# Kernel tuning notes

Hardware: AMD Instinct MI355X
Metric: run time of the kernel (lower is better)

The kernel has to match this reference:

```python
import jax, jax.numpy as jnp
import numpy as np
from jax import lax

T_STEPS = 10       # fixed unroll length in forward (range(10))
TASK = 16          # params['task_size']
FEAT = 256         # input_size - task_size
VOCAB = 128        # params['vocab_size']
SH = 512           # sender_hidden_size
RH = 512           # receiver_hidden_size
ND = 10            # num_digits
B = 16384          # batch_size


def _gru_step(h, x, Wih, Whh, bih, bhh):
    # PyTorch GRU/GRUCell equations. Wih: [3H, In], Whh: [3H, H]
    gi = x @ Wih.T + bih
    gh = h @ Whh.T + bhh
    ir, iz, inn = jnp.split(gi, 3, axis=-1)
    hr, hz, hn = jnp.split(gh, 3, axis=-1)
    r = jax.nn.sigmoid(ir + hr)
    z = jax.nn.sigmoid(iz + hz)
    n = jnp.tanh(inn + r * hn)
    return (1.0 - z) * n + z * h


def setup_inputs() -> dict:
    key = jax.random.key(0)
    ks = jax.random.split(key, 16)
    s = 0.05
    x = jax.random.normal(ks[0], (B, TASK + FEAT), jnp.float32)
    u = jax.random.uniform(ks[1], (T_STEPS, B, VOCAB), jnp.float32, 1e-6, 1.0 - 1e-6)
    gumbel = -jnp.log(-jnp.log(u))  # standard Gumbel noise, fixed for determinism
    inp = {
        "x": x,
        "gumbel": gumbel,
        "W_in": jax.random.normal(ks[2], (SH, FEAT), jnp.float32) * s,
        "b_in": jnp.zeros((SH,), jnp.float32),
        "Wih_s": jax.random.normal(ks[3], (3 * SH, VOCAB), jnp.float32) * s,
        "Whh_s": jax.random.normal(ks[4], (3 * SH, SH), jnp.float32) * s,
        "bih_s": jnp.zeros((3 * SH,), jnp.float32),
        "bhh_s": jnp.zeros((3 * SH,), jnp.float32),
        "W_sp": jax.random.normal(ks[5], (VOCAB, SH), jnp.float32) * s,
        "b_sp": jnp.zeros((VOCAB,), jnp.float32),
        "Wih_r": jax.random.normal(ks[6], (3 * RH, VOCAB), jnp.float32) * s,
        "Whh_r": jax.random.normal(ks[7], (3 * RH, RH), jnp.float32) * s,
        "bih_r": jnp.zeros((3 * RH,), jnp.float32),
        "bhh_r": jnp.zeros((3 * RH,), jnp.float32),
        "W_c": jax.random.normal(ks[8], (ND, RH + TASK), jnp.float32) * s,
        "b_c": jnp.zeros((ND,), jnp.float32),
    }
    return inp


def _forward(x, gumbel, W_in, b_in, Wih_s, Whh_s, bih_s, bhh_s, W_sp, b_sp,
             Wih_r, Whh_r, bih_r, bhh_r, W_c, b_c):
    feats = x[:, TASK:]
    task = x[:, :TASK]
    h0 = jnp.tanh(feats @ W_in.T + b_in)                      # [B, SH]
    inp0 = jnp.zeros((x.shape[0], VOCAB), x.dtype)

    def sender_step(carry, g):
        h, w = carry
        h = _gru_step(h, w, Wih_s, Whh_s, bih_s, bhh_s)
        logits = h @ W_sp.T + b_sp
        y_soft = jax.nn.softmax(logits + g, axis=-1)          # gumbel_softmax, tau=1
        onehot = jax.nn.one_hot(jnp.argmax(y_soft, axis=-1), VOCAB, dtype=y_soft.dtype)
        y = onehot + y_soft - lax.stop_gradient(y_soft)       # hard straight-through
        return (h, lax.stop_gradient(y)), y                   # input_word = y.detach()

    (_, _), output_words = lax.scan(sender_step, (h0, inp0), gumbel)  # [10, B, V]

    # cumulative stop-token masking: once argmax==0 at step i-1, zero all steps >= i
    words = jnp.argmax(output_words, axis=2)                  # [10, B]
    nz = (words != 0).astype(output_words.dtype)
    alive = jnp.concatenate(
        [jnp.ones((1, words.shape[1]), output_words.dtype), jnp.cumprod(nz[:-1], axis=0)],
        axis=0)                                               # [10, B]
    masked = output_words * alive[:, :, None]

    # receiver GRU, zero initial hidden, return final hidden
    hr0 = jnp.zeros((x.shape[0], RH), x.dtype)

    def recv_step(h, w):
        h = _gru_step(h, w, Wih_r, Whh_r, bih_r, bhh_r)
        return h, None

    h_n, _ = lax.scan(recv_step, hr0, masked)                 # [B, RH]
    score = jnp.concatenate([h_n, task], axis=1) @ W_c.T + b_c  # [B, ND]
    return score


def reference(x, gumbel, W_in, b_in, Wih_s, Whh_s, bih_s, bhh_s, W_sp, b_sp,
              Wih_r, Whh_r, bih_r, bhh_r, W_c, b_c):
    return _forward(x, gumbel, W_in, b_in, Wih_s, Whh_s, bih_s, bhh_s, W_sp, b_sp,
                    Wih_r, Whh_r, bih_r, bhh_r, W_c, b_c)
```

## Files before the change

kernel.cpp:

```cpp
#include <hip/hip_runtime.h>
#include <math.h>

#define NB 16384
#define NT 10
#define CHM 8192

typedef _Float16 f16;
typedef f16 f16x8 __attribute__((ext_vector_type(8)));
typedef f16 f16x4 __attribute__((ext_vector_type(4)));
typedef float f32x4 __attribute__((ext_vector_type(4)));

__device__ __forceinline__ float sigm(float v) { return 1.0f / (1.0f + expf(-v)); }

__global__ __launch_bounds__(256) void h0_kernel(
    const float* __restrict__ x, const float* __restrict__ W,
    const float* __restrict__ bias, f16* __restrict__ h_hi, f16* __restrict__ h_lo)
{
    __shared__ __align__(16) float As[32][128];
    __shared__ __align__(16) float Ws[32][64];
    const int t = threadIdx.x;
    const int tx = t & 15, ty = t >> 4;
    const int mBase = blockIdx.x * 128, nBase = blockIdx.y * 64;
    const int kq = (t & 7) * 4, r8 = t >> 3;

    float4 acc[8];
    #pragma unroll
    for (int mi = 0; mi < 8; ++mi) acc[mi] = make_float4(0.f, 0.f, 0.f, 0.f);

    const float* aPtr = x + (size_t)(mBase + r8) * 272 + 16 + kq;
    const float* wPtr = W + (size_t)(nBase + r8) * 256 + kq;

    for (int kb = 0; kb < 8; ++kb) {
        const int k0 = kb * 32;
        __syncthreads();
        #pragma unroll
        for (int i = 0; i < 4; ++i) {
            float4 v = *(const float4*)(aPtr + (size_t)(i * 32) * 272 + k0);
            const int row = r8 + i * 32;
            const float vv[4] = {v.x, v.y, v.z, v.w};
            #pragma unroll
            for (int j = 0; j < 4; ++j) As[kq + j][row ^ ((kq + j) & 28)] = vv[j];
        }
        #pragma unroll
        for (int i = 0; i < 2; ++i) {
            float4 v = *(const float4*)(wPtr + (size_t)(i * 32) * 256 + k0);
            const int row = r8 + i * 32;
            const float vv[4] = {v.x, v.y, v.z, v.w};
            #pragma unroll
            for (int j = 0; j < 4; ++j) Ws[kq + j][row ^ ((kq + j) & 28)] = vv[j];
        }
        __syncthreads();
        #pragma unroll 8
        for (int k = 0; k < 32; ++k) {
            const int s = k & 28;
            float4 a0 = *(const float4*)&As[k][(ty * 8) ^ s];
            float4 a1 = *(const float4*)&As[k][((ty * 8) + 4) ^ s];
            float4 bb = *(const float4*)&Ws[k][(tx * 4) ^ s];
            const float am[8] = {a0.x, a0.y, a0.z, a0.w, a1.x, a1.y, a1.z, a1.w};
            #pragma unroll
            for (int mi = 0; mi < 8; ++mi) {
                acc[mi].x += am[mi] * bb.x; acc[mi].y += am[mi] * bb.y;
                acc[mi].z += am[mi] * bb.z; acc[mi].w += am[mi] * bb.w;
            }
        }
    }
    const int j0 = nBase + tx * 4;
    const int kg = j0 >> 3, jo = j0 & 7;
    const float4 b4 = *(const float4*)&bias[j0];
    #pragma unroll
    for (int mi = 0; mi < 8; ++mi) {
        const int row = mBase + ty * 8 + mi;
        float o[4];
        o[0] = tanhf(acc[mi].x + b4.x); o[1] = tanhf(acc[mi].y + b4.y);
        o[2] = tanhf(acc[mi].z + b4.z); o[3] = tanhf(acc[mi].w + b4.w);
        f16x4 hi4, lo4;
        #pragma unroll
        for (int c = 0; c < 4; ++c) {
            f16 hv = (f16)o[c];
            hi4[c] = hv;
            lo4[c] = (f16)(o[c] - (float)hv);
        }
        *(f16x4*)&h_hi[((size_t)kg * CHM + row) * 8 + jo] = hi4;
        *(f16x4*)&h_lo[((size_t)kg * CHM + row) * 8 + jo] = lo4;
    }
}

__global__ __launch_bounds__(256) void wsplit_kernel(
    const float* __restrict__ W, f16* __restrict__ whi, f16* __restrict__ wlo, int rows)
{
    const int u = blockIdx.x * 256 + threadIdx.x;
    const int kg = u / rows, row = u - kg * rows;
    const float* s = W + (size_t)row * 512 + kg * 8;
    f16x8 hi8, lo8;
    #pragma unroll
    for (int i = 0; i < 8; ++i) {
        float v = s[i];
        f16 hv = (f16)v;
        hi8[i] = hv;
        lo8[i] = (f16)(v - (float)hv);
    }
    *(f16x8*)&whi[(size_t)u * 8] = hi8;
    *(f16x8*)&wlo[(size_t)u * 8] = lo8;
}

__global__ __launch_bounds__(256) void wihT_kernel(
    const float* __restrict__ Wih, float* __restrict__ WihT)
{
    const int u = blockIdx.x * 256 + threadIdx.x;
    const int w = u / 1536, c = u - w * 1536;
    WihT[u] = Wih[(size_t)c * 128 + w];
}

#define INIT_SP() { \
    _Pragma("unroll") \
    for (int i = 0; i < NST; ++i) { \
        const int u = i * 256 + t; \
        const f16* src; \
        if (PURE) { \
            if (u < 512) { \
                src = hc_hi + ((size_t)(u >> 7) * MS + m0 + (u & 127)) * 8; \
            } else { \
                const int w = u - 512; \
                src = w_hi + ((size_t)((w >> 6) & 3) * 1536 + (w >> 8) * 512 + n0 + (w & 63)) * 8; \
            } \
        } else { \
            if (u < 1024) { \
                const int v = u & 511; \
                const f16* hp = (u < 512) ? hc_hi : hc_lo; \
                src = hp + ((size_t)(v >> 7) * MS + m0 + (v & 127)) * 8; \
            } else { \
                const int v = u - 1024; \
                const f16* wp = (v < 768) ? w_hi : w_lo; \
                const int w = (v < 768) ? v : v - 768; \
                src = wp + ((size_t)((w >> 6) & 3) * 1536 + (w >> 8) * 512 + n0 + (w & 63)) * 8; \
            } \
        } \
        sp[i] = src; \
    } \
}
#define LOAD_TILE() { \
    _Pragma("unroll") \
    for (int i = 0; i < NST; ++i) { \
        st[i] = *(const f16x8*)sp[i]; \
        sp[i] += (i < HCNT) ? (size_t)MS * 32 : (size_t)49152; \
    } \
}

template <int HZERO, int PURE>
__global__ __launch_bounds__(256, 2) void fused_gru(
    const f16* __restrict__ hc_hi, const f16* __restrict__ hc_lo,
    f16* __restrict__ hn_hi, f16* __restrict__ hn_lo,
    const f16* __restrict__ w_hi, const f16* __restrict__ w_lo,
    const float* __restrict__ WihT,
    const float* __restrict__ bih, const float* __restrict__ bhh,
    const int* __restrict__ wsel, int MS)
{
    constexpr int UNITS = PURE ? 1280 : 2560;
    constexpr int NST = PURE ? 5 : 10;
    constexpr int HCNT = PURE ? 2 : 4;
    __shared__ __align__(16) f16 lds[2 * UNITS * 8];
    const int t = threadIdx.x;
    const int lane = t & 63, wave = t >> 6;
    const int wm = wave >> 1, wn = wave & 1;
    const int m0 = blockIdx.x * 128;
    const int n0 = blockIdx.y * 64;

    const f32x4 z4 = {0.f, 0.f, 0.f, 0.f};
    f32x4 acc[3][4][2];
    #pragma unroll
    for (int g = 0; g < 3; ++g)
        #pragma unroll
        for (int mi = 0; mi < 4; ++mi)
            #pragma unroll
            for (int ni = 0; ni < 2; ++ni) acc[g][mi][ni] = z4;

    if (!HZERO) {
        const int asel = ((lane >> 4) << 7) + wm * 64 + (lane & 15);
        const int bsel = ((lane >> 4) << 6) + wn * 32 + (lane & 15);
        constexpr int B0 = PURE ? 512 : 1024;

        const f16* sp[NST];
        f16x8 st[NST];
        INIT_SP();
        LOAD_TILE();

        for (int kb = 0; kb < 16; ++kb) {
            f16* lb = lds + (size_t)(kb & 1) * UNITS * 8;
            #pragma unroll
            for (int i = 0; i < NST; ++i)
                *(f16x8*)&lb[(size_t)(i * 256 + t) * 8] = st[i];
            __syncthreads();
            if (kb < 15) LOAD_TILE();

            f16x8 ah[4], al[4];
            #pragma unroll
            for (int mi = 0; mi < 4; ++mi) {
                ah[mi] = *(const f16x8*)&lb[(size_t)(asel + mi * 16) * 8];
                if (!PURE) al[mi] = *(const f16x8*)&lb[(size_t)(512 + asel + mi * 16) * 8];
            }
            #pragma unroll
            for (int g = 0; g < 3; ++g) {
                f16x8 bh[2], bl[2];
                #pragma unroll
                for (int ni = 0; ni < 2; ++ni) {
                    bh[ni] = *(const f16x8*)&lb[(size_t)(B0 + g * 256 + bsel + ni * 16) * 8];
                    if (!PURE) bl[ni] = *(const f16x8*)&lb[(size_t)(1792 + g * 256 + bsel + ni * 16) * 8];
                }
                #pragma unroll
                for (int mi = 0; mi < 4; ++mi)
                    #pragma unroll
                    for (int ni = 0; ni < 2; ++ni) {
                        acc[g][mi][ni] = __builtin_amdgcn_mfma_f32_16x16x32_f16(ah[mi], bh[ni], acc[g][mi][ni], 0, 0, 0);
                        if (!PURE) {
                            acc[g][mi][ni] = __builtin_amdgcn_mfma_f32_16x16x32_f16(ah[mi], bl[ni], acc[g][mi][ni], 0, 0, 0);
                            acc[g][mi][ni] = __builtin_amdgcn_mfma_f32_16x16x32_f16(al[mi], bh[ni], acc[g][mi][ni], 0, 0, 0);
                        }
                    }
            }
        }
    }

    const int colb = n0 + wn * 32 + (lane & 15);
    const int rowb = m0 + wm * 64 + ((lane >> 4) << 2);
    int wd[16];
    #pragma unroll
    for (int mi = 0; mi < 4; ++mi)
        #pragma unroll
        for (int j = 0; j < 4; ++j)
            wd[mi * 4 + j] = wsel ? wsel[rowb + mi * 16 + j] : -1;

    #pragma unroll
    for (int ni = 0; ni < 2; ++ni) {
        const int col = colb + ni * 16;
        const float b_r = bih[col], b_z = bih[512 + col], b_n = bih[1024 + col];
        const float c_r = bhh[col], c_z = bhh[512 + col], c_n = bhh[1024 + col];
        const size_t cbase = (size_t)(col >> 3) * MS * 8 + (col & 7);
        #pragma unroll
        for (int mi = 0; mi < 4; ++mi) {
            #pragma unroll
            for (int j = 0; j < 4; ++j) {
                const int r = rowb + mi * 16 + j;
                const int word = wd[mi * 4 + j];
                float wir = 0.f, wiz = 0.f, win = 0.f;
                if (word >= 0) {
                    const float* wt = WihT + (size_t)word * 1536 + col;
                    wir = wt[0]; wiz = wt[512]; win = wt[1024];
                }
                const size_t idx = cbase + (size_t)r * 8;
                float hold = 0.f;
                if (!HZERO) {
                    hold = (float)hc_hi[idx];
                    if (!PURE) hold += (float)hc_lo[idx];
                }
                const float rr = sigm(wir + b_r + acc[0][mi][ni][j] + c_r);
                const float zz = sigm(wiz + b_z + acc[1][mi][ni][j] + c_z);
                const float nn = tanhf(win + b_n + rr * (acc[2][mi][ni][j] + c_n));
                const float hv = (1.f - zz) * nn + zz * hold;
                const f16 hh = (f16)hv;
                hn_hi[idx] = hh;
                if (!PURE) hn_lo[idx] = (f16)(hv - (float)hh);
            }
        }
    }
}

__global__ __launch_bounds__(256, 2) void argmax_mfma(
    const f16* __restrict__ h0_hi, const f16* __restrict__ h0_lo,
    const f16* __restrict__ h1_hi, const f16* __restrict__ h1_lo,
    const f16* __restrict__ wsp_hi, const f16* __restrict__ wsp_lo,
    const float* __restrict__ bsp, const float* __restrict__ gum,
    int* __restrict__ wout)
{
    __shared__ __align__(16) f16 lds[2 * 1536 * 8];
    const int t = threadIdx.x;
    const int lane = t & 63, wave = t >> 6;
    const int gRow = blockIdx.x * 64;
    const int ch = (gRow >= CHM);
    const int mBase = gRow - ch * CHM;
    const f16* h_hi = ch ? h1_hi : h0_hi;
    const f16* h_lo = ch ? h1_lo : h0_lo;

    const f32x4 z4 = {0.f, 0.f, 0.f, 0.f};
    f32x4 acc[8];
    #pragma unroll
    for (int nf = 0; nf < 8; ++nf) acc[nf] = z4;

    const f16* sp[6];
    sp[0] = h_hi   + ((size_t)(t >> 6) * CHM + mBase + (t & 63)) * 8;
    sp[1] = h_lo   + ((size_t)(t >> 6) * CHM + mBase + (t & 63)) * 8;
    sp[2] = wsp_hi + ((size_t)(t >> 7) * 128 + (t & 127)) * 8;
    sp[3] = wsp_hi + ((size_t)(2 + (t >> 7)) * 128 + (t & 127)) * 8;
    sp[4] = wsp_lo + ((size_t)(t >> 7) * 128 + (t & 127)) * 8;
    sp[5] = wsp_lo + ((size_t)(2 + (t >> 7)) * 128 + (t & 127)) * 8;

    f16x8 st[6];
    #pragma unroll
    for (int i = 0; i < 6; ++i) {
        st[i] = *(const f16x8*)sp[i];
        sp[i] += (i < 2) ? (size_t)CHM * 32 : (size_t)4096;
    }

    const int aselU = (lane >> 4) * 64 + wave * 16 + (lane & 15);
    const int bselU = 512 + (lane >> 4) * 128 + (lane & 15);

    for (int kb = 0; kb < 16; ++kb) {
        f16* lb = lds + (size_t)(kb & 1) * 1536 * 8;
        #pragma unroll
        for (int i = 0; i < 6; ++i)
            *(f16x8*)&lb[(size_t)(i * 256 + t) * 8] = st[i];
        __syncthreads();
        if (kb < 15) {
            #pragma unroll
            for (int i = 0; i < 6; ++i) {
                st[i] = *(const f16x8*)sp[i];
                sp[i] += (i < 2) ? (size_t)CHM * 32 : (size_t)4096;
            }
        }

        f16x8 ah = *(const f16x8*)&lb[(size_t)aselU * 8];
        f16x8 al = *(const f16x8*)&lb[(size_t)(256 + aselU) * 8];
        #pragma unroll
        for (int nf = 0; nf < 8; ++nf) {
            f16x8 bh = *(const f16x8*)&lb[(size_t)(bselU + nf * 16) * 8];
            f16x8 bl = *(const f16x8*)&lb[(size_t)(512 + bselU + nf * 16) * 8];
            acc[nf] = __builtin_amdgcn_mfma_f32_16x16x32_f16(ah, bh, acc[nf], 0, 0, 0);
            acc[nf] = __builtin_amdgcn_mfma_f32_16x16x32_f16(ah, bl, acc[nf], 0, 0, 0);
            acc[nf] = __builtin_amdgcn_mfma_f32_16x16x32_f16(al, bh, acc[nf], 0, 0, 0);
        }
    }

    float bv[4];
    int bi[4];
    #pragma unroll
    for (int j = 0; j < 4; ++j) { bv[j] = -1e30f; bi[j] = 0; }
    const int rw0 = gRow + wave * 16 + ((lane >> 4) << 2);
    #pragma unroll
    for (int nf = 0; nf < 8; ++nf) {
        const int col = (lane & 15) + nf * 16;
        const float bb = bsp[col];
        #pragma unroll
        for (int j = 0; j < 4; ++j) {
            const float v = acc[nf][j] + bb + gum[(size_t)(rw0 + j) * 128 + col];
            if (v > bv[j] || (v == bv[j] && col < bi[j])) { bv[j] = v; bi[j] = col; }
        }
    }
    #pragma unroll
    for (int j = 0; j < 4; ++j) {
        #pragma unroll
        for (int off = 1; off <= 8; off <<= 1) {
            const float ov = __shfl_xor(bv[j], off, 64);
            const int oi = __shfl_xor(bi[j], off, 64);
            if (ov > bv[j] || (ov == bv[j] && oi < bi[j])) { bv[j] = ov; bi[j] = oi; }
        }
        if ((lane & 15) == 0) wout[rw0 + j] = bi[j];
    }
}

__global__ __launch_bounds__(256) void eff_kernel(
    const int* __restrict__ words, int* __restrict__ eff)
{
    const int b = blockIdx.x * 256 + threadIdx.x;
    int alive = 1;
    #pragma unroll
    for (int t = 0; t < NT; ++t) {
        const int w = words[(size_t)t * NB + b];
        eff[(size_t)t * NB + b] = alive ? w : -1;
        alive = alive & (w != 0);
    }
}

__global__ __launch_bounds__(256) void score_kernel(
    const f16* __restrict__ h_hi,
    const float* __restrict__ x, const float* __restrict__ Wc,
    const float* __restrict__ bc, float* __restrict__ out)
{
    __shared__ float Wcs[10][528];
    const int t = threadIdx.x;
    for (int q = t; q < 1320; q += 256)
        *(float4*)&(((float*)Wcs)[q * 4]) = *(const float4*)&Wc[q * 4];
    __syncthreads();

    const int row = blockIdx.x * 256 + t;
    float acc[10];
    #pragma unroll
    for (int d = 0; d < 10; ++d) acc[d] = 0.f;

    for (int kg = 0; kg < 64; ++kg) {
        f16x8 vh = *(const f16x8*)&h_hi[((size_t)kg * NB + row) * 8];
        #pragma unroll
        for (int i = 0; i < 8; ++i) {
            const float v = (float)vh[i];
            #pragma unroll
            for (int d = 0; d < 10; ++d) acc[d] += v * Wcs[d][kg * 8 + i];
        }
    }
    #pragma unroll
    for (int j = 0; j < 16; ++j) {
        const float tv = x[(size_t)row * 272 + j];
        #pragma unroll
        for (int d = 0; d < 10; ++d) acc[d] += tv * Wcs[d][512 + j];
    }
    #pragma unroll
    for (int d = 0; d < 10; ++d) out[(size_t)row * 10 + d] = acc[d] + bc[d];
}

extern "C" void kernel_launch(void* const* d_in, const int* in_sizes, int n_in,
                              void* d_out, int out_size, void* d_ws, size_t ws_size,
                              hipStream_t stream) {
    const float* x      = (const float*)d_in[0];
    const float* gumbel = (const float*)d_in[1];
    const float* W_in   = (const float*)d_in[2];
    const float* b_in   = (const float*)d_in[3];
    const float* Wih_s  = (const float*)d_in[4];
    const float* Whh_s  = (const float*)d_in[5];
    const float* bih_s  = (const float*)d_in[6];
    const float* bhh_s  = (const float*)d_in[7];
    const float* W_sp   = (const float*)d_in[8];
    const float* b_sp   = (const float*)d_in[9];
    const float* Wih_r  = (const float*)d_in[10];
    const float* Whh_r  = (const float*)d_in[11];
    const float* bih_r  = (const float*)d_in[12];
    const float* bhh_r  = (const float*)d_in[13];
    const float* W_c    = (const float*)d_in[14];
    const float* b_c    = (const float*)d_in[15];
    float* out = (float*)d_out;

    char* base = (char*)d_ws;
    f16* cb[3];
    cb[0] = (f16*)(base);
    cb[1] = (f16*)(base + 16777216);
    cb[2] = (f16*)(base + 33554432);
    f16* R0 = (f16*)(base);
    f16* R1 = (f16*)(base + 16777216);
    f16* ws_s_hi = (f16*)(base + 50331648);
    f16* ws_s_lo = (f16*)(base + 51904512);
    f16* ws_r_hi = (f16*)(base + 53477376);
    f16* ws_r_lo = (f16*)(base + 55050240);
    float* wihT_s = (float*)(base + 56623104);
    float* wihT_r = (float*)(base + 57409536);
    int* words   = (int*)(base + 58195968);
    int* eff     = (int*)(base + 58851328);
    f16* wsp_hi  = (f16*)(base + 59506688);
    f16* wsp_lo  = (f16*)(base + 59637760);

    const size_t LOFF = 4194304;
    #define HI(b) (b)
    #define LO(b) ((b) + LOFF)

    const dim3 blk(256);
    const dim3 gFusS(CHM / 128, 8);
    const dim3 gFusR(NB / 128, 8);

    wsplit_kernel<<<dim3(384), blk, 0, stream>>>(Whh_s, ws_s_hi, ws_s_lo, 1536);
    wsplit_kernel<<<dim3(384), blk, 0, stream>>>(Whh_r, ws_r_hi, ws_r_lo, 1536);
    wsplit_kernel<<<dim3(32), blk, 0, stream>>>(W_sp, wsp_hi, wsp_lo, 128);
    wihT_kernel<<<dim3(768), blk, 0, stream>>>(Wih_s, wihT_s);
    wihT_kernel<<<dim3(768), blk, 0, stream>>>(Wih_r, wihT_r);

    h0_kernel<<<gFusS, blk, 0, stream>>>(x, W_in, b_in, HI(cb[0]), LO(cb[0]));
    h0_kernel<<<gFusS, blk, 0, stream>>>(x + (size_t)CHM * 272, W_in, b_in, HI(cb[1]), LO(cb[1]));
    int c0 = 0, c1 = 1, fr = 2;

    for (int t = 0; t < NT; ++t) {
        const int* wprev = (t == 0) ? (const int*)nullptr : (words + (size_t)(t - 1) * NB);
        fused_gru<0, 0><<<gFusS, blk, 0, stream>>>(
            HI(cb[c0]), LO(cb[c0]), HI(cb[fr]), LO(cb[fr]),
            ws_s_hi, ws_s_lo, wihT_s, bih_s, bhh_s, wprev, CHM);
        fused_gru<0, 0><<<gFusS, blk, 0, stream>>>(
            HI(cb[c1]), LO(cb[c1]), HI(cb[c0]), LO(cb[c0]),
            ws_s_hi, ws_s_lo, wihT_s, bih_s, bhh_s,
            wprev ? wprev + CHM : (const int*)nullptr, CHM);
        const int nf = c1; c1 = c0; c0 = fr; fr = nf;
        argmax_mfma<<<dim3(NB / 64), blk, 0, stream>>>(
            HI(cb[c0]), LO(cb[c0]), HI(cb[c1]), LO(cb[c1]), wsp_hi, wsp_lo,
            b_sp, gumbel + (size_t)t * NB * 128, words + (size_t)t * NB);
    }
    eff_kernel<<<dim3(NB / 256), blk, 0, stream>>>(words, eff);

    fused_gru<1, 1><<<gFusR, blk, 0, stream>>>(
        R1, R1, R0, R0, ws_r_hi, ws_r_lo, wihT_r, bih_r, bhh_r, eff, NB);
    for (int t = 1; t < NT; ++t) {
        f16* rin  = (t & 1) ? R0 : R1;
        f16* rout = (t & 1) ? R1 : R0;
        fused_gru<0, 1><<<gFusR, blk, 0, stream>>>(
            rin, rin, rout, rout, ws_r_hi, ws_r_lo, wihT_r, bih_r, bhh_r,
            eff + (size_t)t * NB, NB);
    }

    score_kernel<<<dim3(NB / 256), blk, 0, stream>>>(R1, x, W_c, b_c, out);
}
```

Measured before the change: 1.751 ms.

## Stage GRU tiles with async global-to-LDS loads and use fast activations

Replaces the register-staged double-buffered tile loads in the fused GRU kernel with direct global_load_lds asynchronous copies into the next LDS buffer, moving the barrier to the end of each k-iteration. This removes register staging and the ds_write step and lets the copies overlap the MFMA work. The PURE (fp16-only) variant also swaps expf/tanhf for __expf plus hardware reciprocal approximations, lowering the cost of the elementwise epilogue at some cost in precision. Correctness of the new pipeline depends on the async copies having landed before the trailing barrier, and no explicit vmcnt wait is placed inside the loop.

```diff
diff --git a/kernel.cpp b/kernel.cpp
--- a/kernel.cpp
+++ b/kernel.cpp
@@ -11,6 +11,18 @@
 typedef float f32x4 __attribute__((ext_vector_type(4)));
 
 __device__ __forceinline__ float sigm(float v) { return 1.0f / (1.0f + expf(-v)); }
+__device__ __forceinline__ float sigm_fast(float v) {
+    return __builtin_amdgcn_rcpf(1.0f + __expf(-v));
+}
+__device__ __forceinline__ float tanh_fast(float v) {
+    return 1.0f - 2.0f * __builtin_amdgcn_rcpf(1.0f + __expf(2.0f * v));
+}
+
+__device__ __forceinline__ void async_cp16(const f16* g, f16* l) {
+    __builtin_amdgcn_global_load_lds(
+        (const __attribute__((address_space(1))) unsigned int*)g,
+        (__attribute__((address_space(3))) unsigned int*)l, 16, 0, 0);
+}
 
 __global__ __launch_bounds__(256) void h0_kernel(
     const float* __restrict__ x, const float* __restrict__ W,
@@ -138,10 +150,11 @@
         sp[i] = src; \
     } \
 }
-#define LOAD_TILE() { \
+#define STAGE(buf_) { \
+    f16* lb_ = lds + ((size_t)(buf_) * UNITS + wbase) * 8; \
     _Pragma("unroll") \
     for (int i = 0; i < NST; ++i) { \
-        st[i] = *(const f16x8*)sp[i]; \
+        async_cp16(sp[i], lb_ + (size_t)i * 256 * 8); \
         sp[i] += (i < HCNT) ? (size_t)MS * 32 : (size_t)49152; \
     } \
 }
@@ -164,6 +177,7 @@
     const int wm = wave >> 1, wn = wave & 1;
     const int m0 = blockIdx.x * 128;
     const int n0 = blockIdx.y * 64;
+    const int wbase = t & 192;
 
     const f32x4 z4 = {0.f, 0.f, 0.f, 0.f};
     f32x4 acc[3][4][2];
@@ -180,18 +194,15 @@
         constexpr int B0 = PURE ? 512 : 1024;
 
         const f16* sp[NST];
-        f16x8 st[NST];
         INIT_SP();
-        LOAD_TILE();
+        STAGE(0);
+        asm volatile("s_waitcnt vmcnt(0)" ::: "memory");
+        __syncthreads();
 
         for (int kb = 0; kb < 16; ++kb) {
-            f16* lb = lds + (size_t)(kb & 1) * UNITS * 8;
-            #pragma unroll
-            for (int i = 0; i < NST; ++i)
-                *(f16x8*)&lb[(size_t)(i * 256 + t) * 8] = st[i];
-            __syncthreads();
-            if (kb < 15) LOAD_TILE();
-
+            if (kb < 15) STAGE((kb + 1) & 1);
+
+            const f16* lb = lds + (size_t)(kb & 1) * UNITS * 8;
             f16x8 ah[4], al[4];
             #pragma unroll
             for (int mi = 0; mi < 4; ++mi) {
@@ -217,6 +228,7 @@
                         }
                     }
             }
+            __syncthreads();
         }
     }
 
@@ -252,9 +264,12 @@
                     hold = (float)hc_hi[idx];
                     if (!PURE) hold += (float)hc_lo[idx];
                 }
-                const float rr = sigm(wir + b_r + acc[0][mi][ni][j] + c_r);
-                const float zz = sigm(wiz + b_z + acc[1][mi][ni][j] + c_z);
-                const float nn = tanhf(win + b_n + rr * (acc[2][mi][ni][j] + c_n));
+                const float ra = wir + b_r + acc[0][mi][ni][j] + c_r;
+                const float za = wiz + b_z + acc[1][mi][ni][j] + c_z;
+                const float rr = PURE ? sigm_fast(ra) : sigm(ra);
+                const float zz = PURE ? sigm_fast(za) : sigm(za);
+                const float na = win + b_n + rr * (acc[2][mi][ni][j] + c_n);
+                const float nn = PURE ? tanh_fast(na) : tanhf(na);
                 const float hv = (1.f - zz) * nn + zz * hold;
                 const f16 hh = (f16)hv;
                 hn_hi[idx] = hh;
```

Result: faster. 1.613 ms (-7.9%).
